# Performance work log

Measured on AMD Instinct MI355X. Metric: run time of the kernel, lower is better.

Reference implementation:

```python
import jax, jax.numpy as jnp
import numpy as np

N_NODES = 40000
N_EDGES = 640000
IN_CH = 128
HID = 128
OUT_CH = 16
N_GRAPHS = 64
EPS = 1e-16


def segment_softmax(logits, seg, num_segments):
    m = jax.ops.segment_max(logits, seg, num_segments=num_segments)
    e = jnp.exp(logits - m[seg])
    s = jax.ops.segment_sum(e, seg, num_segments=num_segments)
    return e / (s[seg] + EPS)


def gt_conv(x, src, dst, W, b, att):
    # x: [N, Cin] -> h: [N, C]
    h = x @ W + b
    s = h @ att  # [N] per-node attention score (att broadcast over rows)
    # alpha_e = <x_i, att> + <x_j, att>; x_i = target (dst), x_j = source (src)
    alpha = s[dst] + s[src]
    alpha = jax.nn.leaky_relu(alpha, negative_slope=0.2)
    # PyG code normalizes over edge_index[0] groups (source nodes)
    alpha = segment_softmax(alpha, src, x.shape[0])
    msg = h[src] * alpha[:, None]
    return jax.ops.segment_sum(msg, dst, num_segments=x.shape[0])


def gcn_conv(x, src, dst, W, b):
    n = x.shape[0]
    h = x @ W
    deg = jax.ops.segment_sum(jnp.ones_like(src, dtype=h.dtype), dst, num_segments=n)
    dinv = jnp.where(deg > 0, deg ** -0.5, 0.0)
    norm = dinv[src] * dinv[dst]
    out = jax.ops.segment_sum(h[src] * norm[:, None], dst, num_segments=n)
    return out + b


def setup_inputs() -> dict:
    key = jax.random.key(0)
    ks = jax.random.split(key, 12)
    x = jax.random.normal(ks[0], (N_NODES, IN_CH), dtype=jnp.float32)
    edge_index = jax.random.randint(ks[1], (2, N_EDGES), 0, N_NODES, dtype=jnp.int32)
    batch = jnp.sort(jax.random.randint(ks[2], (N_NODES,), 0, N_GRAPHS, dtype=jnp.int32))
    def glorot(k, shape):
        fan_in, fan_out = shape[0], shape[-1]
        lim = jnp.sqrt(6.0 / (fan_in + fan_out))
        return jax.random.uniform(k, shape, jnp.float32, -lim, lim)
    return {
        "x": x, "edge_index": edge_index, "batch": batch,
        "W1": glorot(ks[3], (IN_CH, HID)), "b1": jnp.zeros((HID,), jnp.float32),
        "att1": glorot(ks[4], (1, HID))[0],
        "W2": glorot(ks[5], (HID, HID)), "b2": jnp.zeros((HID,), jnp.float32),
        "att2": glorot(ks[6], (1, HID))[0],
        "Wg": glorot(ks[7], (HID, HID)), "bg": jnp.zeros((HID,), jnp.float32),
        "Wfc": glorot(ks[8], (HID, OUT_CH)), "bfc": jnp.zeros((OUT_CH,), jnp.float32),
    }


def reference(x, edge_index, batch, W1, b1, att1, W2, b2, att2, Wg, bg, Wfc, bfc):
    n = x.shape[0]
    loops = jnp.arange(n, dtype=edge_index.dtype)
    src = jnp.concatenate([edge_index[0], loops])
    dst = jnp.concatenate([edge_index[1], loops])
    # two GT layers (dropout is identity in eval mode)
    h = jax.nn.relu(gt_conv(x, src, dst, W1, b1, att1))
    h = jax.nn.relu(gt_conv(h, src, dst, W2, b2, att2))
    # GCNConv (with self loops, symmetric normalization)
    h = gcn_conv(h, src, dst, Wg, bg)
    # global mean pool over graphs
    sums = jax.ops.segment_sum(h, batch, num_segments=N_GRAPHS)
    counts = jax.ops.segment_sum(jnp.ones((n,), h.dtype), batch, num_segments=N_GRAPHS)
    pooled = sums / jnp.maximum(counts, 1.0)[:, None]
    logits = pooled @ Wfc + bfc
    return jax.nn.log_softmax(logits, axis=1)
```

## Files before the change

kernel.cpp:

```cpp
#include <hip/hip_runtime.h>
#include <hip/hip_fp16.h>
#include <hip/hip_fp8.h>
#include <math.h>

#define NN 40000
#define NE 640000
#define ET 680000
#define CH 128
#define OC 16
#define NG 64
#define NQ (ET/4)
#define CAP 48
#define NBKT 8
#define BKT_DIV 5000
#define NFILLB 5320
#define NGEMMB 625
#define NGRP 79
#define GRP 72
#define NBLK1 (NGRP*GRP + (NFILLB - NGRP*64))

typedef _Float16 h8 __attribute__((ext_vector_type(8)));
typedef float    f4 __attribute__((ext_vector_type(4)));

__device__ __forceinline__ float2 fp8x2_to_f32(unsigned short v) {
    __hip_fp8_e4m3 a, b;
    a.__x = (__hip_fp8_storage_t)(v & 0xff);
    b.__x = (__hip_fp8_storage_t)(v >> 8);
    return make_float2((float)a, (float)b);
}
__device__ __forceinline__ unsigned char f32_to_fp8(float f) {
    __hip_fp8_e4m3 t(f);
    return (unsigned char)t.__x;
}

__global__ __launch_bounds__(256)
void prep(const int* __restrict__ batch, int* __restrict__ gstart,
          int* __restrict__ cur_d, int* __restrict__ cur_s,
          float* __restrict__ pooled,
          const float* __restrict__ W1, const float* __restrict__ W2,
          const float* __restrict__ Wg, _Float16* __restrict__ Wt1,
          _Float16* __restrict__ Wt2, _Float16* __restrict__ Wtg)
{
    int i = blockIdx.x * 256 + threadIdx.x;
    if (i < NN) {
        cur_d[i] = 0; cur_s[i] = 0;
        int b = batch[i];
        if (i == 0) { for (int g = 0; g <= b; ++g) gstart[g] = 0; }
        else { int pb = batch[i - 1]; for (int g = pb + 1; g <= b; ++g) gstart[g] = i; }
        if (i == NN - 1) { for (int g = b + 1; g <= NG; ++g) gstart[g] = NN; }
    }
    if (i < NG * CH) pooled[i] = 0.f;
    if (i < CH * CH) {
        int k = i >> 7, n = i & 127;
        Wt1[n * CH + k] = (_Float16)W1[i];
        Wt2[n * CH + k] = (_Float16)W2[i];
        Wtg[n * CH + k] = (_Float16)Wg[i];
    }
}

__device__ __forceinline__
void stage_w(_Float16 (*wt)[136], const _Float16* __restrict__ Wt, int tid)
{
#pragma unroll
    for (int i = 0; i < 8; ++i) {
        int f = tid + i * 256;
        int n = f >> 4, c8 = f & 15;
        *(float4*)&wt[n][c8 * 8] = *(const float4*)(Wt + (size_t)n * CH + c8 * 8);
    }
}

template<bool BIAS, bool ATTN>
__device__ __forceinline__
void mfma_body(_Float16 (*xs)[136], _Float16 (*wt)[136],
               const float* __restrict__ bias, const float* __restrict__ att,
               unsigned char* __restrict__ out8, float* __restrict__ s,
               int rb, int tid)
{
    const int wv = tid >> 6, lane = tid & 63;
    const int m = lane & 15, quad = lane >> 4;
    f4 acc[8] = {};
#pragma unroll
    for (int ks = 0; ks < 4; ++ks) {
        h8 a = *(const h8*)&xs[wv * 16 + m][ks * 32 + quad * 8];
#pragma unroll
        for (int t = 0; t < 8; ++t) {
            h8 b = *(const h8*)&wt[t * 16 + m][ks * 32 + quad * 8];
            acc[t] = __builtin_amdgcn_mfma_f32_16x16x32_f16(a, b, acc[t], 0, 0, 0);
        }
    }
    float pr[4] = {0.f, 0.f, 0.f, 0.f};
#pragma unroll
    for (int t = 0; t < 8; ++t) {
        int col = t * 16 + m;
        float bv = BIAS ? bias[col] : 0.f;
        float av = ATTN ? att[col] : 0.f;
#pragma unroll
        for (int r = 0; r < 4; ++r) {
            float o = acc[t][r] + bv;
            int row = rb + wv * 16 + quad * 4 + r;
            out8[(size_t)row * CH + col] = f32_to_fp8(o);
            if (ATTN) pr[r] += o * av;
        }
    }
    if (ATTN) {
#pragma unroll
        for (int r = 0; r < 4; ++r) {
            float p = pr[r];
            p += __shfl_xor(p, 1); p += __shfl_xor(p, 2);
            p += __shfl_xor(p, 4); p += __shfl_xor(p, 8);
            if (m == 0) s[rb + wv * 16 + quad * 4 + r] = p;
        }
    }
}

__device__ __forceinline__
void fill_body(int fb, int tid, const int* __restrict__ ei,
               int* __restrict__ cur_d, int* __restrict__ cur_s,
               unsigned short* __restrict__ pad_src,
               unsigned short* __restrict__ pad_dst)
{
    int bkt = fb & (NBKT - 1);
    int q = (fb >> 3) * 256 + tid;
    if (q >= NQ) return;
    int e0 = q * 4;
    int4 sv, dv;
    if (e0 < NE) {
        sv = *(const int4*)(ei + e0);
        dv = *(const int4*)(ei + NE + e0);
    } else {
        int b = e0 - NE;
        sv = make_int4(b, b + 1, b + 2, b + 3);
        dv = sv;
    }
    const int* sc = (const int*)&sv;
    const int* dc = (const int*)&dv;
#pragma unroll
    for (int u = 0; u < 4; ++u) {
        int srcE = sc[u], dstE = dc[u];
        if ((unsigned)dstE / BKT_DIV == (unsigned)bkt) {
            int p = atomicAdd(cur_d + dstE, 1);
            if (p < CAP) pad_src[dstE * CAP + p] = (unsigned short)srcE;
        }
        if ((unsigned)srcE / BKT_DIV == (unsigned)bkt) {
            int p = atomicAdd(cur_s + srcE, 1);
            if (p < CAP) pad_dst[srcE * CAP + p] = (unsigned short)dstE;
        }
    }
}

__global__ __launch_bounds__(256)
void fill_gemm1(const float* __restrict__ x, const _Float16* __restrict__ Wt1,
                const float* __restrict__ b1, const float* __restrict__ att1,
                unsigned char* __restrict__ out8, float* __restrict__ s1,
                const int* __restrict__ ei, int* __restrict__ cur_d,
                int* __restrict__ cur_s, unsigned short* __restrict__ pad_src,
                unsigned short* __restrict__ pad_dst)
{
    __shared__ __attribute__((aligned(16))) _Float16 xs[64][136];
    __shared__ __attribute__((aligned(16))) _Float16 wt[128][136];
    int grp = blockIdx.x / GRP, o = blockIdx.x % GRP;
    if (grp < NGRP && o < 8) {
        int g = grp * 8 + o;
        if (g < NGEMMB) {
            int rb = g * 64, tid = threadIdx.x;
#pragma unroll
            for (int i = 0; i < 4; ++i) {
                int f = tid + i * 256;
                int r = f >> 4, c8 = f & 15;
                const float* p = x + (size_t)(rb + r) * CH + c8 * 8;
                float4 v0 = *(const float4*)p;
                float4 v1 = *(const float4*)(p + 4);
                __half2 h[4] = { __floats2half2_rn(v0.x, v0.y), __floats2half2_rn(v0.z, v0.w),
                                 __floats2half2_rn(v1.x, v1.y), __floats2half2_rn(v1.z, v1.w) };
                *(float4*)&xs[r][c8 * 8] = *(float4*)h;
            }
            stage_w(wt, Wt1, tid);
            __syncthreads();
            mfma_body<true, true>(xs, wt, b1, att1, out8, s1, rb, tid);
        }
        return;
    }
    int fb = (grp < NGRP) ? grp * 64 + (o - 8)
                          : NGRP * 64 + (blockIdx.x - NGRP * GRP);
    if (fb < NFILLB)
        fill_body(fb, threadIdx.x, ei, cur_d, cur_s, pad_src, pad_dst);
}

template<bool RELU, bool BIAS, bool ATTN>
__global__ __launch_bounds__(256)
void gemm_k(const __half* __restrict__ in, const _Float16* __restrict__ Wt,
            const float* __restrict__ bias, const float* __restrict__ att,
            unsigned char* __restrict__ out8, float* __restrict__ s)
{
    __shared__ __attribute__((aligned(16))) _Float16 xs[64][136];
    __shared__ __attribute__((aligned(16))) _Float16 wt[128][136];
    const int tid = threadIdx.x;
    const int rb = blockIdx.x * 64;
#pragma unroll
    for (int i = 0; i < 4; ++i) {
        int f = tid + i * 256;
        int r = f >> 4, c8 = f & 15;
        float4 raw = *(const float4*)(in + (size_t)(rb + r) * CH + c8 * 8);
        if (RELU) {
            __half2* h2 = (__half2*)&raw;
#pragma unroll
            for (int u = 0; u < 4; ++u) {
                float2 fv = __half22float2(h2[u]);
                h2[u] = __floats2half2_rn(fmaxf(fv.x, 0.f), fmaxf(fv.y, 0.f));
            }
        }
        *(float4*)&xs[r][c8 * 8] = raw;
    }
    stage_w(wt, Wt, tid);
    __syncthreads();
    mfma_body<BIAS, ATTN>(xs, wt, bias, att, out8, s, rb, tid);
}

__global__ __launch_bounds__(256)
void softmax_stats(const int* __restrict__ cur_s,
                   const unsigned short* __restrict__ pad_dst,
                   const float* __restrict__ s, float* __restrict__ ssum)
{
    int node = (blockIdx.x * 256 + threadIdx.x) >> 6;
    int lane = threadIdx.x & 63;
    if (node >= NN) return;
    int deg = min(cur_s[node], CAP);
    float si = s[node];
    float sum = 0.f;
    if (lane < deg) {
        int d = pad_dst[node * CAP + lane];
        float t = si + s[d];
        t = t > 0.f ? t : 0.2f * t;
        sum = expf(t);
    }
#pragma unroll
    for (int o = 32; o; o >>= 1) sum += __shfl_xor(sum, o);
    if (lane == 0) ssum[node] = sum;
}

__device__ __forceinline__
void gather_core(int node, int lane, int deg, int src, float w,
                 const unsigned char* __restrict__ h8p, __half* __restrict__ out16)
{
    int qtr = lane >> 4, cl = lane & 15;
    float a[8] = {};
    for (int base = 0; base < deg; base += 8) {
        uint2 v[2]; float wj[2];
#pragma unroll
        for (int u = 0; u < 2; ++u) {
            int e = base + 4 * u + qtr;
            int sj = __shfl(src, e);
            wj[u]  = __shfl(w, e);
            v[u] = ((const uint2*)(h8p + (size_t)sj * CH))[cl];
        }
#pragma unroll
        for (int u = 0; u < 2; ++u) {
            float2 p0 = fp8x2_to_f32((unsigned short)(v[u].x & 0xffff));
            float2 p1 = fp8x2_to_f32((unsigned short)(v[u].x >> 16));
            float2 p2 = fp8x2_to_f32((unsigned short)(v[u].y & 0xffff));
            float2 p3 = fp8x2_to_f32((unsigned short)(v[u].y >> 16));
            a[0] += p0.x * wj[u]; a[1] += p0.y * wj[u];
            a[2] += p1.x * wj[u]; a[3] += p1.y * wj[u];
            a[4] += p2.x * wj[u]; a[5] += p2.y * wj[u];
            a[6] += p3.x * wj[u]; a[7] += p3.y * wj[u];
        }
    }
#pragma unroll
    for (int k = 0; k < 8; ++k) {
        a[k] += __shfl_xor(a[k], 16);
        a[k] += __shfl_xor(a[k], 32);
    }
    if (qtr == 0) {
        float4 st;
        ((__half2*)&st)[0] = __floats2half2_rn(a[0], a[1]);
        ((__half2*)&st)[1] = __floats2half2_rn(a[2], a[3]);
        ((__half2*)&st)[2] = __floats2half2_rn(a[4], a[5]);
        ((__half2*)&st)[3] = __floats2half2_rn(a[6], a[7]);
        ((float4*)(out16 + (size_t)node * CH))[cl] = st;
    }
}

__global__ __launch_bounds__(256)
void gt_gather(const int* __restrict__ cur_d,
               const unsigned short* __restrict__ pad_src,
               const unsigned char* __restrict__ h8p, const float* __restrict__ s,
               const float* __restrict__ ssum, __half* __restrict__ out16)
{
    int node = (blockIdx.x * 256 + threadIdx.x) >> 6;
    int lane = threadIdx.x & 63;
    if (node >= NN) return;
    int deg = min(cur_d[node], CAP);
    float sd = s[node];
    int src = 0; float w = 0.f;
    if (lane < deg) {
        src = pad_src[node * CAP + lane];
        float t = sd + s[src];
        t = t > 0.f ? t : 0.2f * t;
        w = expf(t) / ssum[src];
    }
    gather_core(node, lane, deg, src, w, h8p, out16);
}

__global__ __launch_bounds__(256)
void gcn_gather(const int* __restrict__ cur_d,
                const unsigned short* __restrict__ pad_src,
                const unsigned char* __restrict__ h8p, __half* __restrict__ out16)
{
    int node = (blockIdx.x * 256 + threadIdx.x) >> 6;
    int lane = threadIdx.x & 63;
    if (node >= NN) return;
    int dn = cur_d[node];
    int deg = min(dn, CAP);
    float nu = rsqrtf((float)max(dn, 1));
    int src = 0; float w = 0.f;
    if (lane < deg) {
        src = pad_src[node * CAP + lane];
        w = rsqrtf((float)max(cur_d[src], 1)) * nu;
    }
    gather_core(node, lane, deg, src, w, h8p, out16);
}

__global__ __launch_bounds__(128)
void pool_part(const __half* __restrict__ h16, const int* __restrict__ batch,
               float* __restrict__ pooled)
{
    int ch = threadIdx.x;
    int start = blockIdx.x * 80;
    float acc = 0.f;
    int curg = batch[start];
    for (int base = start; base < start + 80; base += 8) {
        float vals[8]; int gs[8];
#pragma unroll
        for (int u = 0; u < 8; ++u)
            vals[u] = __half2float(h16[(size_t)(base + u) * CH + ch]);
#pragma unroll
        for (int u = 0; u < 8; ++u) gs[u] = batch[base + u];
#pragma unroll
        for (int u = 0; u < 8; ++u) {
            if (gs[u] != curg) {
                atomicAdd(pooled + (size_t)curg * CH + ch, acc);
                acc = 0.f; curg = gs[u];
            }
            acc += vals[u];
        }
    }
    atomicAdd(pooled + (size_t)curg * CH + ch, acc);
}

__global__ __launch_bounds__(256)
void head_kernel(const float* __restrict__ psum, const int* __restrict__ gstart,
                 const float* __restrict__ bg, const float* __restrict__ Wfc,
                 const float* __restrict__ bfc, float* __restrict__ out)
{
    __shared__ float lg[NG][OC];
    int tid = threadIdx.x;
#pragma unroll
    for (int i = 0; i < 4; ++i) {
        int f = tid + i * 256;
        int g = f >> 4, o = f & 15;
        float cnt = fmaxf((float)(gstart[g + 1] - gstart[g]), 1.0f);
        float inv = 1.0f / cnt;
        float acc = bfc[o];
        for (int c = 0; c < CH; ++c)
            acc += (psum[g * CH + c] * inv + bg[c]) * Wfc[c * OC + o];
        lg[g][o] = acc;
    }
    __syncthreads();
    if (tid < NG) {
        float m = -1e30f;
#pragma unroll
        for (int o = 0; o < OC; ++o) m = fmaxf(m, lg[tid][o]);
        float sum = 0.f;
#pragma unroll
        for (int o = 0; o < OC; ++o) sum += expf(lg[tid][o] - m);
        float lse = m + logf(sum);
#pragma unroll
        for (int o = 0; o < OC; ++o) out[tid * OC + o] = lg[tid][o] - lse;
    }
}

extern "C" void kernel_launch(void* const* d_in, const int* in_sizes, int n_in,
                              void* d_out, int out_size, void* d_ws, size_t ws_size,
                              hipStream_t stream)
{
    const float* x     = (const float*)d_in[0];
    const int*   ei    = (const int*)d_in[1];
    const int*   batch = (const int*)d_in[2];
    const float* W1    = (const float*)d_in[3];
    const float* b1    = (const float*)d_in[4];
    const float* att1  = (const float*)d_in[5];
    const float* W2    = (const float*)d_in[6];
    const float* b2    = (const float*)d_in[7];
    const float* att2  = (const float*)d_in[8];
    const float* Wg    = (const float*)d_in[9];
    const float* bg    = (const float*)d_in[10];
    const float* Wfc   = (const float*)d_in[11];
    const float* bfc   = (const float*)d_in[12];
    float* out = (float*)d_out;

    const size_t NNCH = (size_t)NN * CH;
    __half* B16 = (__half*)d_ws;
    unsigned char* A8 = (unsigned char*)(B16 + NNCH);
    _Float16* Wt1 = (_Float16*)(A8 + NNCH);
    _Float16* Wt2 = Wt1 + CH * CH;
    _Float16* Wtg = Wt2 + CH * CH;
    int*   cur_d  = (int*)(Wtg + CH * CH);
    int*   cur_s  = cur_d + NN;
    float* s1     = (float*)(cur_s + NN);
    float* s2     = s1 + NN;
    float* pooled = s2 + NN;
    float* ssum   = pooled + NG * CH;
    int*   gstart = (int*)(ssum + NN);
    unsigned short* pad_src = (unsigned short*)(gstart + NG + 1);
    unsigned short* pad_dst = pad_src + (size_t)NN * CAP;

    const int WB = NN / 4;

    prep<<<157, 256, 0, stream>>>(batch, gstart, cur_d, cur_s, pooled,
                                  W1, W2, Wg, Wt1, Wt2, Wtg);

    fill_gemm1<<<NBLK1, 256, 0, stream>>>(
        x, Wt1, b1, att1, A8, s1, ei, cur_d, cur_s, pad_src, pad_dst);
    softmax_stats<<<WB, 256, 0, stream>>>(cur_s, pad_dst, s1, ssum);
    gt_gather<<<WB, 256, 0, stream>>>(cur_d, pad_src, A8, s1, ssum, B16);

    gemm_k<true, true, true><<<NGEMMB, 256, 0, stream>>>(
        B16, Wt2, b2, att2, A8, s2);
    softmax_stats<<<WB, 256, 0, stream>>>(cur_s, pad_dst, s2, ssum);
    gt_gather<<<WB, 256, 0, stream>>>(cur_d, pad_src, A8, s2, ssum, B16);

    gemm_k<true, false, false><<<NGEMMB, 256, 0, stream>>>(
        B16, Wtg, nullptr, nullptr, A8, nullptr);
    gcn_gather<<<WB, 256, 0, stream>>>(cur_d, pad_src, A8, B16);

    pool_part<<<500, 128, 0, stream>>>(B16, batch, pooled);
    head_kernel<<<1, 256, 0, stream>>>(pooled, gstart, bg, Wfc, bfc, out);
}
```

Baseline: 277.7 us.

## Pad degree counters per cacheline, preload gather rows, fuse pool with head

```diff
diff --git a/kernel.cpp b/kernel.cpp
--- a/kernel.cpp
+++ b/kernel.cpp
@@ -18,6 +18,8 @@
 #define NGRP 79
 #define GRP 72
 #define NBLK1 (NGRP*GRP + (NFILLB - NGRP*64))
+#define CSTR 16
+#define NPOOL 500
 
 typedef _Float16 h8 __attribute__((ext_vector_type(8)));
 typedef float    f4 __attribute__((ext_vector_type(4)));
@@ -35,21 +37,20 @@
 
 __global__ __launch_bounds__(256)
 void prep(const int* __restrict__ batch, int* __restrict__ gstart,
-          int* __restrict__ cur_d, int* __restrict__ cur_s,
-          float* __restrict__ pooled,
+          float* __restrict__ pooled, int* __restrict__ done,
           const float* __restrict__ W1, const float* __restrict__ W2,
           const float* __restrict__ Wg, _Float16* __restrict__ Wt1,
           _Float16* __restrict__ Wt2, _Float16* __restrict__ Wtg)
 {
     int i = blockIdx.x * 256 + threadIdx.x;
     if (i < NN) {
-        cur_d[i] = 0; cur_s[i] = 0;
         int b = batch[i];
         if (i == 0) { for (int g = 0; g <= b; ++g) gstart[g] = 0; }
         else { int pb = batch[i - 1]; for (int g = pb + 1; g <= b; ++g) gstart[g] = i; }
         if (i == NN - 1) { for (int g = b + 1; g <= NG; ++g) gstart[g] = NN; }
     }
     if (i < NG * CH) pooled[i] = 0.f;
+    if (i == 0) done[0] = 0;
     if (i < CH * CH) {
         int k = i >> 7, n = i & 127;
         Wt1[n * CH + k] = (_Float16)W1[i];
@@ -138,11 +139,11 @@
     for (int u = 0; u < 4; ++u) {
         int srcE = sc[u], dstE = dc[u];
         if ((unsigned)dstE / BKT_DIV == (unsigned)bkt) {
-            int p = atomicAdd(cur_d + dstE, 1);
+            int p = atomicAdd(cur_d + (size_t)dstE * CSTR, 1);
             if (p < CAP) pad_src[dstE * CAP + p] = (unsigned short)srcE;
         }
         if ((unsigned)srcE / BKT_DIV == (unsigned)bkt) {
-            int p = atomicAdd(cur_s + srcE, 1);
+            int p = atomicAdd(cur_s + (size_t)srcE * CSTR, 1);
             if (p < CAP) pad_dst[srcE * CAP + p] = (unsigned short)dstE;
         }
     }
@@ -224,7 +225,7 @@
     int node = (blockIdx.x * 256 + threadIdx.x) >> 6;
     int lane = threadIdx.x & 63;
     if (node >= NN) return;
-    int deg = min(cur_s[node], CAP);
+    int deg = min(cur_s[(size_t)node * CSTR], CAP);
     float si = s[node];
     float sum = 0.f;
     if (lane < deg) {
@@ -243,26 +244,36 @@
                  const unsigned char* __restrict__ h8p, __half* __restrict__ out16)
 {
     int qtr = lane >> 4, cl = lane & 15;
+    int nb = (deg + 7) >> 3;
+    uint2 v[12]; float wj[12];
+#pragma unroll
+    for (int b = 0; b < 6; ++b) {
+        if (b < nb) {
+#pragma unroll
+            for (int u = 0; u < 2; ++u) {
+                int e = b * 8 + 4 * u + qtr;
+                int sj = __shfl(src, e);
+                wj[b * 2 + u] = __shfl(w, e);
+                v[b * 2 + u] = ((const uint2*)(h8p + (size_t)sj * CH))[cl];
+            }
+        }
+    }
     float a[8] = {};
-    for (int base = 0; base < deg; base += 8) {
-        uint2 v[2]; float wj[2];
-#pragma unroll
-        for (int u = 0; u < 2; ++u) {
-            int e = base + 4 * u + qtr;
-            int sj = __shfl(src, e);
-            wj[u]  = __shfl(w, e);
-            v[u] = ((const uint2*)(h8p + (size_t)sj * CH))[cl];
-        }
-#pragma unroll
-        for (int u = 0; u < 2; ++u) {
-            float2 p0 = fp8x2_to_f32((unsigned short)(v[u].x & 0xffff));
-            float2 p1 = fp8x2_to_f32((unsigned short)(v[u].x >> 16));
-            float2 p2 = fp8x2_to_f32((unsigned short)(v[u].y & 0xffff));
-            float2 p3 = fp8x2_to_f32((unsigned short)(v[u].y >> 16));
-            a[0] += p0.x * wj[u]; a[1] += p0.y * wj[u];
-            a[2] += p1.x * wj[u]; a[3] += p1.y * wj[u];
-            a[4] += p2.x * wj[u]; a[5] += p2.y * wj[u];
-            a[6] += p3.x * wj[u]; a[7] += p3.y * wj[u];
+#pragma unroll
+    for (int b = 0; b < 6; ++b) {
+        if (b < nb) {
+#pragma unroll
+            for (int u = 0; u < 2; ++u) {
+                int idx = b * 2 + u;
+                float2 p0 = fp8x2_to_f32((unsigned short)(v[idx].x & 0xffff));
+                float2 p1 = fp8x2_to_f32((unsigned short)(v[idx].x >> 16));
+                float2 p2 = fp8x2_to_f32((unsigned short)(v[idx].y & 0xffff));
+                float2 p3 = fp8x2_to_f32((unsigned short)(v[idx].y >> 16));
+                a[0] += p0.x * wj[idx]; a[1] += p0.y * wj[idx];
+                a[2] += p1.x * wj[idx]; a[3] += p1.y * wj[idx];
+                a[4] += p2.x * wj[idx]; a[5] += p2.y * wj[idx];
+                a[6] += p3.x * wj[idx]; a[7] += p3.y * wj[idx];
+            }
         }
     }
 #pragma unroll
@@ -289,7 +300,7 @@
     int node = (blockIdx.x * 256 + threadIdx.x) >> 6;
     int lane = threadIdx.x & 63;
     if (node >= NN) return;
-    int deg = min(cur_d[node], CAP);
+    int deg = min(cur_d[(size_t)node * CSTR], CAP);
     float sd = s[node];
     int src = 0; float w = 0.f;
     if (lane < deg) {
@@ -309,21 +320,27 @@
     int node = (blockIdx.x * 256 + threadIdx.x) >> 6;
     int lane = threadIdx.x & 63;
     if (node >= NN) return;
-    int dn = cur_d[node];
+    int dn = cur_d[(size_t)node * CSTR];
     int deg = min(dn, CAP);
     float nu = rsqrtf((float)max(dn, 1));
     int src = 0; float w = 0.f;
     if (lane < deg) {
         src = pad_src[node * CAP + lane];
-        w = rsqrtf((float)max(cur_d[src], 1)) * nu;
+        w = rsqrtf((float)max(cur_d[(size_t)src * CSTR], 1)) * nu;
     }
     gather_core(node, lane, deg, src, w, h8p, out16);
 }
 
 __global__ __launch_bounds__(128)
-void pool_part(const __half* __restrict__ h16, const int* __restrict__ batch,
-               float* __restrict__ pooled)
-{
+void pool_head(const __half* __restrict__ h16, const int* __restrict__ batch,
+               float* __restrict__ pooled, int* __restrict__ done,
+               const int* __restrict__ gstart, const float* __restrict__ bg,
+               const float* __restrict__ Wfc, const float* __restrict__ bfc,
+               float* __restrict__ out)
+{
+    __shared__ float sp[NG][CH];
+    __shared__ float lg[NG][OC];
+    __shared__ int sh_last;
     int ch = threadIdx.x;
     int start = blockIdx.x * 80;
     float acc = 0.f;
@@ -345,37 +362,42 @@
         }
     }
     atomicAdd(pooled + (size_t)curg * CH + ch, acc);
-}
-
-__global__ __launch_bounds__(256)
-void head_kernel(const float* __restrict__ psum, const int* __restrict__ gstart,
-                 const float* __restrict__ bg, const float* __restrict__ Wfc,
-                 const float* __restrict__ bfc, float* __restrict__ out)
-{
-    __shared__ float lg[NG][OC];
-    int tid = threadIdx.x;
-#pragma unroll
-    for (int i = 0; i < 4; ++i) {
-        int f = tid + i * 256;
+    __threadfence();
+    if (ch == 0) {
+        int old = __hip_atomic_fetch_add(done, 1, __ATOMIC_ACQ_REL,
+                                         __HIP_MEMORY_SCOPE_AGENT);
+        sh_last = (old == NPOOL - 1);
+    }
+    __syncthreads();
+    if (!sh_last) return;
+    for (int i = 0; i < NG * CH / 128; ++i) {
+        int f = ch + i * 128;
+        ((float*)sp)[f] = __hip_atomic_load(&pooled[f], __ATOMIC_RELAXED,
+                                            __HIP_MEMORY_SCOPE_AGENT);
+    }
+    __syncthreads();
+#pragma unroll
+    for (int i = 0; i < 8; ++i) {
+        int f = ch + i * 128;
         int g = f >> 4, o = f & 15;
         float cnt = fmaxf((float)(gstart[g + 1] - gstart[g]), 1.0f);
         float inv = 1.0f / cnt;
-        float acc = bfc[o];
+        float a = bfc[o];
         for (int c = 0; c < CH; ++c)
-            acc += (psum[g * CH + c] * inv + bg[c]) * Wfc[c * OC + o];
-        lg[g][o] = acc;
+            a += (sp[g][c] * inv + bg[c]) * Wfc[c * OC + o];
+        lg[g][o] = a;
     }
     __syncthreads();
-    if (tid < NG) {
+    if (ch < NG) {
         float m = -1e30f;
 #pragma unroll
-        for (int o = 0; o < OC; ++o) m = fmaxf(m, lg[tid][o]);
+        for (int o = 0; o < OC; ++o) m = fmaxf(m, lg[ch][o]);
         float sum = 0.f;
 #pragma unroll
-        for (int o = 0; o < OC; ++o) sum += expf(lg[tid][o] - m);
+        for (int o = 0; o < OC; ++o) sum += expf(lg[ch][o] - m);
         float lse = m + logf(sum);
 #pragma unroll
-        for (int o = 0; o < OC; ++o) out[tid * OC + o] = lg[tid][o] - lse;
+        for (int o = 0; o < OC; ++o) out[ch * OC + o] = lg[ch][o] - lse;
     }
 }
 
@@ -405,18 +427,20 @@
     _Float16* Wt2 = Wt1 + CH * CH;
     _Float16* Wtg = Wt2 + CH * CH;
     int*   cur_d  = (int*)(Wtg + CH * CH);
-    int*   cur_s  = cur_d + NN;
-    float* s1     = (float*)(cur_s + NN);
+    int*   cur_s  = cur_d + (size_t)NN * CSTR;
+    float* s1     = (float*)(cur_s + (size_t)NN * CSTR);
     float* s2     = s1 + NN;
     float* pooled = s2 + NN;
-    float* ssum   = pooled + NG * CH;
+    int*   done   = (int*)(pooled + NG * CH);
+    float* ssum   = (float*)(done + 1);
     int*   gstart = (int*)(ssum + NN);
     unsigned short* pad_src = (unsigned short*)(gstart + NG + 1);
     unsigned short* pad_dst = pad_src + (size_t)NN * CAP;
 
     const int WB = NN / 4;
 
-    prep<<<157, 256, 0, stream>>>(batch, gstart, cur_d, cur_s, pooled,
+    hipMemsetAsync(cur_d, 0, (size_t)2 * NN * CSTR * 4, stream);
+    prep<<<157, 256, 0, stream>>>(batch, gstart, pooled, done,
                                   W1, W2, Wg, Wt1, Wt2, Wtg);
 
     fill_gemm1<<<NBLK1, 256, 0, stream>>>(
@@ -433,6 +457,6 @@
         B16, Wtg, nullptr, nullptr, A8, nullptr);
     gcn_gather<<<WB, 256, 0, stream>>>(cur_d, pad_src, A8, B16);
 
-    pool_part<<<500, 128, 0, stream>>>(B16, batch, pooled);
-    head_kernel<<<1, 256, 0, stream>>>(pooled, gstart, bg, Wfc, bfc, out);
-}
+    pool_head<<<NPOOL, 128, 0, stream>>>(B16, batch, pooled, done,
+                                         gstart, bg, Wfc, bfc, out);
+}
```

Result: slower. 322.8 us (+16.2%).
